# Kernel tuning notes

Measured on AMD Instinct MI355X. Metric: run time of the kernel, lower is better.

The kernel has to match this reference:

```python
import jax, jax.numpy as jnp
import numpy as np

B, L, D, OUT, EXP = 4, 4096, 128, 55, 2
D2 = 2 * D

def _ln(x, g, b):
    m = jnp.mean(x, axis=-1, keepdims=True)
    v = jnp.mean((x - m) ** 2, axis=-1, keepdims=True)
    return (x - m) / jnp.sqrt(v + 1e-5) * g + b

def setup_inputs() -> dict:
    key = jax.random.key(0)
    ks = iter(jax.random.split(key, 32))
    w = lambda shape: jax.random.normal(next(ks), shape, jnp.float32) * 0.02
    inp = {
        'x1': jax.random.normal(next(ks), (B, L, D), jnp.float32),
        'x2': jax.random.normal(next(ks), (B, L, D), jnp.float32),
        'ln1_g': jnp.ones((D,)), 'ln1_b': jnp.zeros((D,)),
        'ln2_g': jnp.ones((D,)), 'ln2_b': jnp.zeros((D,)),
        'Wq': w((D, D)), 'bq': jnp.zeros((D,)),
        'Wv1': w((D, D)), 'bv1': jnp.zeros((D,)),
        'Wk': w((D, D)), 'bk': jnp.zeros((D,)),
        'Wv2': w((D, D)), 'bv2': jnp.zeros((D,)),
        'Wp1': w((D, D)), 'bp1': jnp.zeros((D,)),
        'Wp2': w((D, D)), 'bp2': jnp.zeros((D,)),
        'lnf_g': jnp.ones((D2,)), 'lnf_b': jnp.zeros((D2,)),
        'Wf1': w((D2, EXP * D2)), 'bf1': jnp.zeros((EXP * D2,)),
        'Wf2': w((EXP * D2, D2)), 'bf2': jnp.zeros((D2,)),
        'ln3_g': jnp.ones((D2,)), 'ln3_b': jnp.zeros((D2,)),
        'Wo': w((D2, OUT)), 'bo': jnp.zeros((OUT,)),
    }
    return inp

def reference(x1, x2, ln1_g, ln1_b, ln2_g, ln2_b, Wq, bq, Wv1, bv1, Wk, bk,
              Wv2, bv2, Wp1, bp1, Wp2, bp2, lnf_g, lnf_b, Wf1, bf1, Wf2, bf2,
              ln3_g, ln3_b, Wo, bo):
    res1, res2 = x1, x2
    x1n = _ln(x1, ln1_g, ln1_b)
    x2n = _ln(x2, ln2_g, ln2_b)
    q1 = x1n @ Wq + bq        # [B,L,D]
    v1 = x1n @ Wv1 + bv1
    k2 = x2n @ Wk + bk
    v2 = x2n @ Wv2 + bv2
    # faithful to torch: energy = einsum('bqd,bkd->bqk', keys2, queries1)
    energy = jnp.einsum('bqd,bkd->bqk', k2, q1)
    att = jax.nn.softmax(energy / jnp.sqrt(jnp.float32(D)), axis=-1)  # [B,L,L]
    out1 = jnp.einsum('bal,blv->bav', att, v1) @ Wp1 + bp1
    out2 = jnp.einsum('bal,blv->bav', att, v2) @ Wp2 + bp2
    y1 = out1 + res1
    y2 = out2 + res2
    x = jnp.concatenate([y1, y2], axis=-1)  # [B,L,2D]
    res = x
    h = _ln(x, lnf_g, lnf_b)
    h = jax.nn.gelu(h @ Wf1 + bf1, approximate=False) @ Wf2 + bf2
    x = _ln(h + res, ln3_g, ln3_b)
    return x @ Wo + bo  # [B,L,OUT]
```

## Files before the change

### kernel.cpp

```cpp
#include <hip/hip_runtime.h>
#include <hip/hip_fp16.h>

typedef _Float16 half8 __attribute__((ext_vector_type(8)));
typedef float f32x4 __attribute__((ext_vector_type(4)));
typedef long lng2 __attribute__((ext_vector_type(2)));

#define B_   4
#define L_   4096
#define D_   128
#define M_   (B_*L_)
#define D2_  256
#define H_   512
#define OUT_ 55

__device__ __forceinline__ f32x4 mfma16(half8 a, half8 b, f32x4 c) {
    return __builtin_amdgcn_mfma_f32_16x16x32_f16(a, b, c, 0, 0, 0);
}
__device__ __forceinline__ f32x4 mfma8(long a, long b, f32x4 c) {
    return __builtin_amdgcn_mfma_f32_16x16x32_fp8_fp8(a, b, c, 0, 0, 0);
}
__device__ __forceinline__ int pk4(float a, float b, float c, float d) {
    int t = __builtin_amdgcn_cvt_pk_fp8_f32(a, b, 0, false);
    return __builtin_amdgcn_cvt_pk_fp8_f32(c, d, t, true);
}
__device__ __forceinline__ float fexp2(float x) { return __builtin_amdgcn_exp2f(x); }

#define KSCL (0.08838834764831845f * 1.4426950408889634f)

#define WQ_OFF   0
#define WV1_OFF  16384
#define WK_OFF   32768
#define WV2_OFF  49152
#define WP1_OFF  65536
#define WP2_OFF  81920
#define WF1_OFF  98304
#define WF2_OFF  229376
#define WO_OFF   360448


__global__ void prep_kernel(const float* Wq, const float* Wv1, const float* Wk,
                            const float* Wv2, const float* Wp1, const float* Wp2,
                            const float* Wf1, const float* Wf2, const float* Wo,
                            _Float16* wsw) {
    int id = blockIdx.y;
    int t  = blockIdx.x * 256 + threadIdx.x;
    const float* src = nullptr; int K = 0, N = 0, Npad = 0, off = 0;
    switch (id) {
        case 0: src = Wq;  K = 128; N = 128; Npad = 128; off = WQ_OFF;  break;
        case 1: src = Wv1; K = 128; N = 128; Npad = 128; off = WV1_OFF; break;
        case 2: src = Wk;  K = 128; N = 128; Npad = 128; off = WK_OFF;  break;
        case 3: src = Wv2; K = 128; N = 128; Npad = 128; off = WV2_OFF; break;
        case 4: src = Wp1; K = 128; N = 128; Npad = 128; off = WP1_OFF; break;
        case 5: src = Wp2; K = 128; N = 128; Npad = 128; off = WP2_OFF; break;
        case 6: src = Wf1; K = 256; N = 512; Npad = 512; off = WF1_OFF; break;
        case 7: src = Wf2; K = 512; N = 256; Npad = 256; off = WF2_OFF; break;
        case 8: src = Wo;  K = 256; N = 55;  Npad = 64;  off = WO_OFF;  break;
        default: return;
    }
    int total = K * Npad;
    if (t >= total) return;
    int k = t / Npad, n = t % Npad;
    float v = (n < N) ? src[k * N + n] : 0.f;
    int s = k >> 5, c = n >> 4, ln = n & 15;
    int q, j;
    if (id == 4 || id == 5) { q = (k >> 2) & 3; j = (k & 3) + (((k >> 4) & 1) << 2); }
    else                    { q = (k >> 3) & 3; j = k & 7; }
    int nc = Npad >> 4;
    wsw[off + ((size_t)((s * nc + c) * 64 + q * 16 + ln)) * 8 + j] = (_Float16)v;
}


__global__ __launch_bounds__(256) void ln_kernel(const float* x1, const float* x2,
        const float* g1, const float* b1, const float* g2, const float* b2,
        _Float16* x1n, _Float16* x2n) {
    int wave = threadIdx.x >> 6, lane = threadIdx.x & 63;
    int token = blockIdx.x * 4 + wave;
    const float* x = blockIdx.y ? x2 : x1;
    const float* g = blockIdx.y ? g2 : g1;
    const float* bb = blockIdx.y ? b2 : b1;
    _Float16* o = blockIdx.y ? x2n : x1n;
    const float* xr = x + (size_t)token * D_;
    float a0 = xr[lane], a1 = xr[lane + 64];
    float s = a0 + a1, s2 = a0 * a0 + a1 * a1;
    #pragma unroll
    for (int off = 1; off < 64; off <<= 1) {
        s += __shfl_xor(s, off);
        s2 += __shfl_xor(s2, off);
    }
    float mean = s * (1.f / 128.f);
    float var = s2 * (1.f / 128.f) - mean * mean;
    float inv = rsqrtf(var + 1e-5f);
    int lt = token >> 4, ln_r = token & 15;
    #pragma unroll
    for (int h = 0; h < 2; h++) {
        int col = lane + h * 64;
        float v = (h ? a1 : a0);
        float out = (v - mean) * inv * g[col] + bb[col];
        int ss = col >> 5, q = (col >> 3) & 3, j = col & 7;
        o[((size_t)((lt * 4 + ss) * 64 + q * 16 + ln_r)) * 8 + j] = (_Float16)out;
    }
}

__global__ __launch_bounds__(256) void proj_kernel(const _Float16* x1n, const _Float16* x2n,
        const _Float16* wsw, const float* bq, const float* bv1, const float* bk,
        const float* bv2, _Float16* q1, _Float16* k2, unsigned char* vsw8) {
    int g = blockIdx.y;
    const _Float16* A = (g < 2) ? x1n : x2n;
    const _Float16* Bw = wsw + g * 16384;
    const float* bias = (g == 0) ? bq : (g == 1) ? bv1 : (g == 2) ? bk : bv2;
    int wave = threadIdx.x >> 6, lane = threadIdx.x & 63;
    int quad = lane >> 4, ln = lane & 15;
    int mbase = blockIdx.x * 64 + wave * 16;
    int lt = mbase >> 4;

    half8 a[4];
    #pragma unroll
    for (int s = 0; s < 4; s++)
        a[s] = *(const half8*)(A + ((size_t)((lt * 4 + s) * 64 + lane)) * 8);

    f32x4 acc[8];
    #pragma unroll
    for (int c = 0; c < 8; c++) acc[c] = f32x4{0.f, 0.f, 0.f, 0.f};

    half8 Wc[4], Wn[4];
    #pragma unroll
    for (int s = 0; s < 4; s++)
        Wc[s] = *(const half8*)(Bw + ((size_t)((s * 8 + 0) * 64 + lane)) * 8);
    #pragma unroll
    for (int c = 0; c < 8; c++) {
        int cn = (c < 7) ? c + 1 : 7;
        #pragma unroll
        for (int s = 0; s < 4; s++)
            Wn[s] = *(const half8*)(Bw + ((size_t)((s * 8 + cn) * 64 + lane)) * 8);
        #pragma unroll
        for (int s = 0; s < 4; s++)
            acc[c] = mfma16(a[s], Wc[s], acc[c]);
        #pragma unroll
        for (int s = 0; s < 4; s++) Wc[s] = Wn[s];
    }

    bool isV = (g == 1) || (g == 3);
    if (!isV) {
        float scl = (g == 2) ? KSCL : 1.f;
        _Float16* out = (g == 0) ? q1 : k2;
        #pragma unroll
        for (int c = 0; c < 8; c++) {
            int n = c * 16 + ln;
            float bv = bias[n];
            #pragma unroll
            for (int r = 0; r < 4; r++) {
                int s_o = c >> 1, q_o = ((c & 1) << 1) | (ln >> 3), j = ln & 7;
                out[((size_t)((lt * 4 + s_o) * 64 + q_o * 16 + (quad * 4 + r))) * 8 + j]
                    = (_Float16)((acc[c][r] + bv) * scl);
            }
        }
    } else {
        int cbase = (g == 3) ? 8 : 0;
        int b = mbase >> 12;
        int l0 = (mbase & (L_ - 1)) + quad * 4;
        int sp = l0 >> 6, tt = (l0 >> 4) & 3, q2 = (l0 >> 2) & 3;
        unsigned char* Vb = vsw8 + (size_t)b * (1u << 20);
        #pragma unroll
        for (int c = 0; c < 8; c++) {
            int n = c * 16 + ln;
            float bv = bias[n];
            int pk = pk4(acc[c][0] + bv, acc[c][1] + bv, acc[c][2] + bv, acc[c][3] + bv);
            *(int*)(Vb + (((size_t)(sp * 16 + cbase + c) * 64 + q2 * 16 + ln) * 16 + tt * 4)) = pk;
        }
    }
}

__global__ __launch_bounds__(256) void zero_kernel(float* rowsum) {
    int i = (blockIdx.x * 256 + threadIdx.x) * 4;
    *(f32x4*)(rowsum + i) = f32x4{0.f, 0.f, 0.f, 0.f};
}

__global__ __launch_bounds__(256) void score_kernel(
        const _Float16* __restrict__ q1sw, const _Float16* __restrict__ k2sw,
        unsigned char* __restrict__ pmat8, float* __restrict__ rowsum) {
    int w = threadIdx.x >> 6, lane = threadIdx.x & 63;
    int quad = lane >> 4, ln = lane & 15;
    int b = blockIdx.z;
    int kL0 = blockIdx.y * 128 + (w & 1) * 64;
    int mL0 = blockIdx.x * 128 + (w >> 1) * 64;
    int ltk = ((b << 12) + kL0) >> 4;
    int ltm = ((b << 12) + mL0) >> 4;

    f32x4 acc[4][4];
    #pragma unroll
    for (int i = 0; i < 4; i++)
        #pragma unroll
        for (int j = 0; j < 4; j++) acc[i][j] = f32x4{0.f, 0.f, 0.f, 0.f};

    #pragma unroll
    for (int s = 0; s < 4; s++) {
        half8 a[4], bq[4];
        #pragma unroll
        for (int i = 0; i < 4; i++)
            a[i] = *(const half8*)(q1sw + ((size_t)(((ltk + i) * 4 + s) * 64 + lane)) * 8);
        #pragma unroll
        for (int j = 0; j < 4; j++)
            bq[j] = *(const half8*)(k2sw + ((size_t)(((ltm + j) * 4 + s) * 64 + lane)) * 8);
        #pragma unroll
        for (int i = 0; i < 4; i++)
            #pragma unroll
            for (int j = 0; j < 4; j++)
                acc[i][j] = mfma16(a[i], bq[j], acc[i][j]);
    }

    unsigned char* Pb = pmat8 + (size_t)b * (16u << 20);
    int sp = kL0 >> 6;
    #pragma unroll
    for (int j = 0; j < 4; j++) {
        int4 d;
        float csum = 0.f;
        #pragma unroll
        for (int i = 0; i < 4; i++) {
            float p0 = fexp2(acc[i][j][0]);
            float p1 = fexp2(acc[i][j][1]);
            float p2 = fexp2(acc[i][j][2]);
            float p3 = fexp2(acc[i][j][3]);
            csum += (p0 + p1) + (p2 + p3);
            ((int*)&d)[i] = pk4(p0, p1, p2, p3);
        }
        csum += __shfl_xor(csum, 16);
        csum += __shfl_xor(csum, 32);
        if (lane < 16)
            atomicAdd(&rowsum[(b << 12) + mL0 + j * 16 + ln], csum);
        int lt = (mL0 >> 4) + j;
        *(int4*)(Pb + (((size_t)(lt * 64 + sp)) * 64 + lane) * 16) = d;
    }
}

__global__ __launch_bounds__(256) void pv_kernel(
        const unsigned char* __restrict__ pmat8, const unsigned char* __restrict__ vsw8,
        const float* __restrict__ rowsum,
        _Float16* __restrict__ att1, _Float16* __restrict__ att2) {
    int w = threadIdx.x >> 6, lane = threadIdx.x & 63;
    int quad = lane >> 4, ln = lane & 15;
    int rowG0 = blockIdx.x * 32;
    int b = rowG0 >> 12;
    int lt0 = (rowG0 & (L_ - 1)) >> 4;
    const unsigned char* Pb = pmat8 + (size_t)b * (16u << 20);
    const unsigned char* Vb = vsw8 + (size_t)b * (1u << 20);

    f32x4 acc[4][2];
    #pragma unroll
    for (int i = 0; i < 4; i++)
        #pragma unroll
        for (int c = 0; c < 2; c++) acc[i][c] = f32x4{0.f, 0.f, 0.f, 0.f};

    lng2 Vf[2][4], Pf[2][2];
    #pragma unroll
    for (int p = 0; p < 2; p++) {
        #pragma unroll
        for (int i = 0; i < 4; i++)
            Vf[p][i] = *(const lng2*)(Vb + (((size_t)(p * 16 + w * 4 + i)) * 64 + lane) * 16);
        #pragma unroll
        for (int c = 0; c < 2; c++)
            Pf[p][c] = *(const lng2*)(Pb + (((size_t)((lt0 + c) * 64 + p)) * 64 + lane) * 16);
    }

    #define PVSTEP(buf, sp) do {                                                     \
        int spn = ((sp) + 2 < 64) ? (sp) + 2 : 63;                                   \
        lng2 Vn[4], Pn[2];                                                           \
        _Pragma("unroll")                                                            \
        for (int i = 0; i < 4; i++)                                                  \
            Vn[i] = *(const lng2*)(Vb + (((size_t)(spn * 16 + w * 4 + i)) * 64 + lane) * 16); \
        _Pragma("unroll")                                                            \
        for (int c = 0; c < 2; c++)                                                  \
            Pn[c] = *(const lng2*)(Pb + (((size_t)((lt0 + c) * 64 + spn)) * 64 + lane) * 16); \
        _Pragma("unroll")                                                            \
        for (int i = 0; i < 4; i++)                                                  \
            _Pragma("unroll")                                                        \
            for (int c = 0; c < 2; c++) {                                            \
                acc[i][c] = mfma8(Vf[buf][i].x, Pf[buf][c].x, acc[i][c]);             \
                acc[i][c] = mfma8(Vf[buf][i].y, Pf[buf][c].y, acc[i][c]);             \
            }                                                                        \
        _Pragma("unroll")                                                            \
        for (int i = 0; i < 4; i++) Vf[buf][i] = Vn[i];                              \
        _Pragma("unroll")                                                            \
        for (int c = 0; c < 2; c++) Pf[buf][c] = Pn[c];                              \
    } while (0)

    for (int sp = 0; sp < 64; sp += 2) {
        PVSTEP(0, sp);
        PVSTEP(1, sp + 1);
    }
    #undef PVSTEP

    _Float16* att = (w >= 2) ? att2 : att1;
    #pragma unroll
    for (int c = 0; c < 2; c++) {
        float inv = 1.f / rowsum[rowG0 + c * 16 + ln];
        int lt = (rowG0 >> 4) + c;
        #pragma unroll
        for (int sl = 0; sl < 2; sl++) {
            half8 v;
            #pragma unroll
            for (int r = 0; r < 4; r++) {
                v[r]     = (_Float16)(acc[2 * sl][c][r] * inv);
                v[r + 4] = (_Float16)(acc[2 * sl + 1][c][r] * inv);
            }
            int s = (w & 1) * 2 + sl;
            *(half8*)(att + ((size_t)((lt * 4 + s) * 64 + lane)) * 8) = v;
        }
    }
}

__global__ __launch_bounds__(256) void attn_out_kernel(const _Float16* att1, const _Float16* att2,
        const _Float16* wsw, const float* bp1, const float* bp2,
        const float* x1, const float* x2, const float* lnf_g, const float* lnf_b,
        _Float16* res, _Float16* xn) {
    int wave = threadIdx.x >> 6, lane = threadIdx.x & 63;
    int quad = lane >> 4, ln = lane & 15;
    int mbase = blockIdx.x * 64 + wave * 16;
    int lt = mbase >> 4;
    const _Float16* Wp1 = wsw + WP1_OFF;
    const _Float16* Wp2 = wsw + WP2_OFF;

    half8 a1[4], a2[4];
    #pragma unroll
    for (int s = 0; s < 4; s++) {
        a1[s] = *(const half8*)(att1 + ((size_t)((lt * 4 + s) * 64 + lane)) * 8);
        a2[s] = *(const half8*)(att2 + ((size_t)((lt * 4 + s) * 64 + lane)) * 8);
    }
    f32x4 y1[8], y2[8];
    #pragma unroll
    for (int c = 0; c < 8; c++) { y1[c] = f32x4{0,0,0,0}; y2[c] = f32x4{0,0,0,0}; }

    half8 W1c[4], W2c[4], W1n[4], W2n[4];
    #pragma unroll
    for (int s = 0; s < 4; s++) {
        W1c[s] = *(const half8*)(Wp1 + ((size_t)((s * 8 + 0) * 64 + lane)) * 8);
        W2c[s] = *(const half8*)(Wp2 + ((size_t)((s * 8 + 0) * 64 + lane)) * 8);
    }
    #pragma unroll
    for (int c = 0; c < 8; c++) {
        int cn = (c < 7) ? c + 1 : 7;
        #pragma unroll
        for (int s = 0; s < 4; s++) {
            W1n[s] = *(const half8*)(Wp1 + ((size_t)((s * 8 + cn) * 64 + lane)) * 8);
            W2n[s] = *(const half8*)(Wp2 + ((size_t)((s * 8 + cn) * 64 + lane)) * 8);
        }
        #pragma unroll
        for (int s = 0; s < 4; s++) {
            y1[c] = mfma16(a1[s], W1c[s], y1[c]);
            y2[c] = mfma16(a2[s], W2c[s], y2[c]);
        }
        #pragma unroll
        for (int s = 0; s < 4; s++) { W1c[s] = W1n[s]; W2c[s] = W2n[s]; }
    }

    #pragma unroll
    for (int c = 0; c < 8; c++) {
        int n = c * 16 + ln;
        float b1v = bp1[n], b2v = bp2[n];
        #pragma unroll
        for (int r = 0; r < 4; r++) {
            int m = mbase + quad * 4 + r;
            y1[c][r] += b1v + x1[(size_t)m * D_ + n];
            y2[c][r] += b2v + x2[(size_t)m * D_ + n];
        }
    }
    float sum[4] = {0,0,0,0}, sq[4] = {0,0,0,0};
    #pragma unroll
    for (int c = 0; c < 8; c++)
        #pragma unroll
        for (int r = 0; r < 4; r++) {
            sum[r] += y1[c][r] + y2[c][r];
            sq[r]  += y1[c][r] * y1[c][r] + y2[c][r] * y2[c][r];
        }
    #pragma unroll
    for (int off = 1; off < 16; off <<= 1)
        #pragma unroll
        for (int r = 0; r < 4; r++) { sum[r] += __shfl_xor(sum[r], off); sq[r] += __shfl_xor(sq[r], off); }
    #pragma unroll
    for (int r = 0; r < 4; r++) {
        float mean = sum[r] * (1.f / 256.f);
        float var = sq[r] * (1.f / 256.f) - mean * mean;
        float inv = rsqrtf(var + 1e-5f);
        int m = mbase + quad * 4 + r;
        int lt_m = m >> 4;
        #pragma unroll
        for (int c = 0; c < 8; c++) {
            int n = c * 16 + ln;
            res[(size_t)m * D2_ + n]       = (_Float16)y1[c][r];
            res[(size_t)m * D2_ + 128 + n] = (_Float16)y2[c][r];
            float yn1 = (y1[c][r] - mean) * inv * lnf_g[n] + lnf_b[n];
            float yn2 = (y2[c][r] - mean) * inv * lnf_g[128 + n] + lnf_b[128 + n];
            int s_x = n >> 5, q_x = (n >> 3) & 3, j = n & 7;
            xn[((size_t)((lt_m * 8 + s_x) * 64 + q_x * 16 + (m & 15))) * 8 + j] = (_Float16)yn1;
            int n2 = 128 + n;
            int s_y = n2 >> 5, q_y = (n2 >> 3) & 3, j2 = n2 & 7;
            xn[((size_t)((lt_m * 8 + s_y) * 64 + q_y * 16 + (m & 15))) * 8 + j2] = (_Float16)yn2;
        }
    }
}

__global__ __launch_bounds__(256) void ffn1_kernel(const _Float16* xn, const _Float16* wsw,
        const float* bf1, _Float16* h) {
    int wave = threadIdx.x >> 6, lane = threadIdx.x & 63;
    int quad = lane >> 4, ln = lane & 15;
    int mbase = blockIdx.x * 64 + wave * 16;
    int lt = mbase >> 4;
    int nt = blockIdx.y;
    const _Float16* W = wsw + WF1_OFF;

    half8 a[8];
    #pragma unroll
    for (int s = 0; s < 8; s++)
        a[s] = *(const half8*)(xn + ((size_t)((lt * 8 + s) * 64 + lane)) * 8);

    f32x4 acc[8];
    #pragma unroll
    for (int c = 0; c < 8; c++) acc[c] = f32x4{0,0,0,0};

    half8 Wc[8], Wn[8];
    #pragma unroll
    for (int s = 0; s < 8; s++)
        Wc[s] = *(const half8*)(W + ((size_t)((s * 32 + nt * 8) * 64 + lane)) * 8);
    #pragma unroll
    for (int c = 0; c < 8; c++) {
        int cn = (c < 7) ? c + 1 : 7;
        #pragma unroll
        for (int s = 0; s < 8; s++)
            Wn[s] = *(const half8*)(W + ((size_t)((s * 32 + nt * 8 + cn) * 64 + lane)) * 8);
        #pragma unroll
        for (int s = 0; s < 8; s++)
            acc[c] = mfma16(a[s], Wc[s], acc[c]);
        #pragma unroll
        for (int s = 0; s < 8; s++) Wc[s] = Wn[s];
    }
    #pragma unroll
    for (int c = 0; c < 8; c++) {
        int n = nt * 128 + c * 16 + ln;
        float bv = bf1[n];
        int s_h = n >> 5, q_h = (n >> 3) & 3, j = n & 7;
        #pragma unroll
        for (int r = 0; r < 4; r++) {
            float v = acc[c][r] + bv;
            float u = 0.7978845608f * (v + 0.044715f * v * v * v);
            float e = fexp2(-2.8853900818f * u);
            float ge = v * __builtin_amdgcn_rcpf(1.f + e);
            h[((size_t)((lt * 16 + s_h) * 64 + q_h * 16 + (quad * 4 + r))) * 8 + j] = (_Float16)ge;
        }
    }
}

__global__ __launch_bounds__(256) void ffn2_kernel(const _Float16* h, const _Float16* wsw,
        const float* bf2, const _Float16* res, const float* g3, const float* b3, _Float16* xn2) {
    __shared__ float sst[2][16][2][2];
    int w = threadIdx.x >> 6, lane = threadIdx.x & 63;
    int quad = lane >> 4, ln = lane & 15;
    int rt = w & 1, nh = w >> 1;
    int mb = blockIdx.x * 32 + rt * 16;
    int lt = mb >> 4;
    const _Float16* W = wsw + WF2_OFF;

    f32x4 acc[8];
    #pragma unroll
    for (int c = 0; c < 8; c++) acc[c] = f32x4{0,0,0,0};

    half8 aC, aN;
    half8 Wc[8], Wn[8];
    aC = *(const half8*)(h + ((size_t)((lt * 16 + 0) * 64 + lane)) * 8);
    #pragma unroll
    for (int c = 0; c < 8; c++)
        Wc[c] = *(const half8*)(W + ((size_t)((0 * 16 + nh * 8 + c) * 64 + lane)) * 8);

    #pragma unroll
    for (int s = 0; s < 16; s++) {
        int sn = (s < 15) ? s + 1 : 15;
        aN = *(const half8*)(h + ((size_t)((lt * 16 + sn) * 64 + lane)) * 8);
        #pragma unroll
        for (int c = 0; c < 8; c++)
            Wn[c] = *(const half8*)(W + ((size_t)((sn * 16 + nh * 8 + c) * 64 + lane)) * 8);
        #pragma unroll
        for (int c = 0; c < 8; c++)
            acc[c] = mfma16(aC, Wc[c], acc[c]);
        aC = aN;
        #pragma unroll
        for (int c = 0; c < 8; c++) Wc[c] = Wn[c];
    }

    float y[8][4];
    float psum[4] = {0,0,0,0}, psq[4] = {0,0,0,0};
    #pragma unroll
    for (int c = 0; c < 8; c++) {
        int n = nh * 128 + c * 16 + ln;
        float bv = bf2[n];
        #pragma unroll
        for (int r = 0; r < 4; r++) {
            int m = mb + quad * 4 + r;
            float v = acc[c][r] + bv + (float)res[(size_t)m * D2_ + n];
            y[c][r] = v; psum[r] += v; psq[r] += v * v;
        }
    }
    #pragma unroll
    for (int off = 1; off < 16; off <<= 1)
        #pragma unroll
        for (int r = 0; r < 4; r++) { psum[r] += __shfl_xor(psum[r], off); psq[r] += __shfl_xor(psq[r], off); }
    if (ln == 0)
        #pragma unroll
        for (int r = 0; r < 4; r++) { sst[rt][quad * 4 + r][nh][0] = psum[r]; sst[rt][quad * 4 + r][nh][1] = psq[r]; }
    __syncthreads();
    #pragma unroll
    for (int r = 0; r < 4; r++) {
        float su = sst[rt][quad * 4 + r][0][0] + sst[rt][quad * 4 + r][1][0];
        float sq = sst[rt][quad * 4 + r][0][1] + sst[rt][quad * 4 + r][1][1];
        float mean = su * (1.f / 256.f);
        float var = sq * (1.f / 256.f) - mean * mean;
        float invs = rsqrtf(var + 1e-5f);
        #pragma unroll
        for (int c = 0; c < 8; c++) {
            int n = nh * 128 + c * 16 + ln;
            float yn = (y[c][r] - mean) * invs * g3[n] + b3[n];
            int s_x = n >> 5, q_x = (n >> 3) & 3, j = n & 7;
            xn2[((size_t)((lt * 8 + s_x) * 64 + q_x * 16 + (quad * 4 + r))) * 8 + j] = (_Float16)yn;
        }
    }
}

__global__ __launch_bounds__(256) void out_kernel(const _Float16* xn2, const _Float16* wsw,
        const float* bo, float* out) {
    __shared__ f32x4 pc[2][4][64];
    int w = threadIdx.x >> 6, lane = threadIdx.x & 63;
    int quad = lane >> 4, ln = lane & 15;
    int rt = w & 1, kh = w >> 1;
    int mb = blockIdx.x * 32 + rt * 16;
    int lt = mb >> 4;
    const _Float16* W = wsw + WO_OFF;

    f32x4 acc[4];
    #pragma unroll
    for (int c = 0; c < 4; c++) acc[c] = f32x4{0,0,0,0};
    #pragma unroll
    for (int ss = 0; ss < 4; ss++) {
        int s = kh * 4 + ss;
        half8 a = *(const half8*)(xn2 + ((size_t)((lt * 8 + s) * 64 + lane)) * 8);
        #pragma unroll
        for (int c = 0; c < 4; c++)
            acc[c] = mfma16(a, *(const half8*)(W + ((size_t)((s * 4 + c) * 64 + lane)) * 8), acc[c]);
    }
    if (kh == 1)
        #pragma unroll
        for (int c = 0; c < 4; c++) pc[rt][c][lane] = acc[c];
    __syncthreads();
    if (kh == 0) {
        #pragma unroll
        for (int c = 0; c < 4; c++) {
            f32x4 p = pc[rt][c][lane];
            int n = c * 16 + ln;
            if (n < OUT_) {
                float bv = bo[n];
                #pragma unroll
                for (int r = 0; r < 4; r++)
                    out[(size_t)(mb + quad * 4 + r) * OUT_ + n] = acc[c][r] + p[r] + bv;
            }
        }
    }
}

extern "C" void kernel_launch(void* const* d_in, const int* in_sizes, int n_in,
                              void* d_out, int out_size, void* d_ws, size_t ws_size,
                              hipStream_t stream) {
    const float* x1    = (const float*)d_in[0];
    const float* x2    = (const float*)d_in[1];
    const float* ln1_g = (const float*)d_in[2];
    const float* ln1_b = (const float*)d_in[3];
    const float* ln2_g = (const float*)d_in[4];
    const float* ln2_b = (const float*)d_in[5];
    const float* Wq    = (const float*)d_in[6];
    const float* bq    = (const float*)d_in[7];
    const float* Wv1   = (const float*)d_in[8];
    const float* bv1   = (const float*)d_in[9];
    const float* Wk    = (const float*)d_in[10];
    const float* bk    = (const float*)d_in[11];
    const float* Wv2   = (const float*)d_in[12];
    const float* bv2   = (const float*)d_in[13];
    const float* Wp1   = (const float*)d_in[14];
    const float* bp1   = (const float*)d_in[15];
    const float* Wp2   = (const float*)d_in[16];
    const float* bp2   = (const float*)d_in[17];
    const float* lnf_g = (const float*)d_in[18];
    const float* lnf_b = (const float*)d_in[19];
    const float* Wf1   = (const float*)d_in[20];
    const float* bf1   = (const float*)d_in[21];
    const float* Wf2   = (const float*)d_in[22];
    const float* bf2   = (const float*)d_in[23];
    const float* ln3_g = (const float*)d_in[24];
    const float* ln3_b = (const float*)d_in[25];
    const float* Wo    = (const float*)d_in[26];
    const float* bo    = (const float*)d_in[27];
    float* out = (float*)d_out;

    char* ws = (char*)d_ws;
    const size_t MB = 1 << 20;
    _Float16* q1sw   = (_Float16*)(ws + 0 * MB);
    _Float16* k2sw   = (_Float16*)(ws + 4 * MB);
    unsigned char* vsw8 = (unsigned char*)(ws + 8 * MB);
    _Float16* att1   = (_Float16*)(ws + 12 * MB);
    _Float16* att2   = (_Float16*)(ws + 16 * MB);
    _Float16* x1n    = (_Float16*)(ws + 20 * MB);
    _Float16* x2n    = (_Float16*)(ws + 24 * MB);
    _Float16* wsw    = (_Float16*)(ws + 28 * MB);
    float*    rowsum = (float*)   (ws + 29 * MB);
    _Float16* res    = (_Float16*)(ws + 30 * MB);
    _Float16* xn     = (_Float16*)(ws + 46 * MB);
    _Float16* h      = (_Float16*)(ws + 54 * MB);
    _Float16* xn2    = (_Float16*)(ws + 70 * MB);
    unsigned char* pmat8 = (unsigned char*)(ws + 78 * MB);

    prep_kernel<<<dim3(512, 9), 256, 0, stream>>>(Wq, Wv1, Wk, Wv2, Wp1, Wp2, Wf1, Wf2, Wo, wsw);
    ln_kernel<<<dim3(M_ / 4, 2), 256, 0, stream>>>(x1, x2, ln1_g, ln1_b, ln2_g, ln2_b, x1n, x2n);
    proj_kernel<<<dim3(M_ / 64, 4), 256, 0, stream>>>(x1n, x2n, wsw, bq, bv1, bk, bv2,
                                                      q1sw, k2sw, vsw8);
    zero_kernel<<<dim3(16), 256, 0, stream>>>(rowsum);
    score_kernel<<<dim3(32, 32, 4), 256, 0, stream>>>(q1sw, k2sw, pmat8, rowsum);
    pv_kernel<<<dim3(M_ / 32), 256, 0, stream>>>(pmat8, vsw8, rowsum, att1, att2);
    attn_out_kernel<<<dim3(M_ / 64), 256, 0, stream>>>(att1, att2, wsw, bp1, bp2,
                                                       x1, x2, lnf_g, lnf_b, res, xn);
    ffn1_kernel<<<dim3(M_ / 64, 4), 256, 0, stream>>>(xn, wsw, bf1, h);
    ffn2_kernel<<<dim3(M_ / 32), 256, 0, stream>>>(h, wsw, bf2, res, ln3_g, ln3_b, xn2);
    out_kernel<<<dim3(M_ / 32), 256, 0, stream>>>(xn2, wsw, bo, out);
}
```

Measured before the change: 249.6 us.

## Split PV reduction across wave halves and split attn_out by stream

pv_kernel now launches 512 threads per block. Two groups of four waves each cover half of the key dimension, and the partial accumulators are combined through shared memory before normalization and the store. attn_out_kernel assigns each wave a single stream (att1 or att2) over 16 rows, doubling the grid, and combines the layernorm statistics across waves through shared memory. Both changes aim to raise parallelism and occupancy on the memory-bound stages, at the cost of extra LDS traffic and a block-wide barrier.

```diff
diff --git a/kernel.cpp b/kernel.cpp
--- a/kernel.cpp
+++ b/kernel.cpp
@@ -232,17 +232,21 @@
     }
 }
 
-__global__ __launch_bounds__(256) void pv_kernel(
+__global__ __launch_bounds__(512) void pv_kernel(
         const unsigned char* __restrict__ pmat8, const unsigned char* __restrict__ vsw8,
         const float* __restrict__ rowsum,
         _Float16* __restrict__ att1, _Float16* __restrict__ att2) {
+    __shared__ f32x4 part[4][2][4][64];
     int w = threadIdx.x >> 6, lane = threadIdx.x & 63;
     int quad = lane >> 4, ln = lane & 15;
+    int wc = w & 3, kh = w >> 2;
     int rowG0 = blockIdx.x * 32;
     int b = rowG0 >> 12;
     int lt0 = (rowG0 & (L_ - 1)) >> 4;
     const unsigned char* Pb = pmat8 + (size_t)b * (16u << 20);
     const unsigned char* Vb = vsw8 + (size_t)b * (1u << 20);
+    int c0 = wc * 4;
+    int sp0 = kh * 32;
 
     f32x4 acc[4][2];
     #pragma unroll
@@ -255,18 +259,18 @@
     for (int p = 0; p < 2; p++) {
         #pragma unroll
         for (int i = 0; i < 4; i++)
-            Vf[p][i] = *(const lng2*)(Vb + (((size_t)(p * 16 + w * 4 + i)) * 64 + lane) * 16);
+            Vf[p][i] = *(const lng2*)(Vb + (((size_t)((sp0 + p) * 16 + c0 + i)) * 64 + lane) * 16);
         #pragma unroll
         for (int c = 0; c < 2; c++)
-            Pf[p][c] = *(const lng2*)(Pb + (((size_t)((lt0 + c) * 64 + p)) * 64 + lane) * 16);
-    }
-
-    #define PVSTEP(buf, sp) do {                                                     \
-        int spn = ((sp) + 2 < 64) ? (sp) + 2 : 63;                                   \
+            Pf[p][c] = *(const lng2*)(Pb + (((size_t)((lt0 + c) * 64 + sp0 + p)) * 64 + lane) * 16);
+    }
+
+    #define PVSTEP(buf, ii) do {                                                     \
+        int spn = sp0 + ((((ii) + 2) < 32) ? (ii) + 2 : 31);                         \
         lng2 Vn[4], Pn[2];                                                           \
         _Pragma("unroll")                                                            \
         for (int i = 0; i < 4; i++)                                                  \
-            Vn[i] = *(const lng2*)(Vb + (((size_t)(spn * 16 + w * 4 + i)) * 64 + lane) * 16); \
+            Vn[i] = *(const lng2*)(Vb + (((size_t)(spn * 16 + c0 + i)) * 64 + lane) * 16); \
         _Pragma("unroll")                                                            \
         for (int c = 0; c < 2; c++)                                                  \
             Pn[c] = *(const lng2*)(Pb + (((size_t)((lt0 + c) * 64 + spn)) * 64 + lane) * 16); \
@@ -283,27 +287,43 @@
         for (int c = 0; c < 2; c++) Pf[buf][c] = Pn[c];                              \
     } while (0)
 
-    for (int sp = 0; sp < 64; sp += 2) {
-        PVSTEP(0, sp);
-        PVSTEP(1, sp + 1);
+    for (int ii = 0; ii < 32; ii += 2) {
+        PVSTEP(0, ii);
+        PVSTEP(1, ii + 1);
     }
     #undef PVSTEP
 
-    _Float16* att = (w >= 2) ? att2 : att1;
-    #pragma unroll
-    for (int c = 0; c < 2; c++) {
-        float inv = 1.f / rowsum[rowG0 + c * 16 + ln];
-        int lt = (rowG0 >> 4) + c;
-        #pragma unroll
-        for (int sl = 0; sl < 2; sl++) {
-            half8 v;
+    if (kh == 1) {
+        #pragma unroll
+        for (int i = 0; i < 4; i++)
             #pragma unroll
-            for (int r = 0; r < 4; r++) {
-                v[r]     = (_Float16)(acc[2 * sl][c][r] * inv);
-                v[r + 4] = (_Float16)(acc[2 * sl + 1][c][r] * inv);
+            for (int c = 0; c < 2; c++)
+                part[wc][c][i][lane] = acc[i][c];
+    }
+    __syncthreads();
+    if (kh == 0) {
+        #pragma unroll
+        for (int i = 0; i < 4; i++)
+            #pragma unroll
+            for (int c = 0; c < 2; c++)
+                acc[i][c] += part[wc][c][i][lane];
+
+        _Float16* att = (wc >= 2) ? att2 : att1;
+        #pragma unroll
+        for (int c = 0; c < 2; c++) {
+            float inv = 1.f / rowsum[rowG0 + c * 16 + ln];
+            int lt = (rowG0 >> 4) + c;
+            #pragma unroll
+            for (int sl = 0; sl < 2; sl++) {
+                half8 v;
+                #pragma unroll
+                for (int r = 0; r < 4; r++) {
+                    v[r]     = (_Float16)(acc[2 * sl][c][r] * inv);
+                    v[r + 4] = (_Float16)(acc[2 * sl + 1][c][r] * inv);
+                }
+                int s = (wc & 1) * 2 + sl;
+                *(half8*)(att + ((size_t)((lt * 4 + s) * 64 + lane)) * 8) = v;
             }
-            int s = (w & 1) * 2 + sl;
-            *(half8*)(att + ((size_t)((lt * 4 + s) * 64 + lane)) * 8) = v;
         }
     }
 }
@@ -312,88 +332,82 @@
         const _Float16* wsw, const float* bp1, const float* bp2,
         const float* x1, const float* x2, const float* lnf_g, const float* lnf_b,
         _Float16* res, _Float16* xn) {
-    int wave = threadIdx.x >> 6, lane = threadIdx.x & 63;
+    __shared__ float sst[2][16][2][2];
+    int w = threadIdx.x >> 6, lane = threadIdx.x & 63;
     int quad = lane >> 4, ln = lane & 15;
-    int mbase = blockIdx.x * 64 + wave * 16;
+    int rt = w & 1, st = w >> 1;
+    int mbase = blockIdx.x * 32 + rt * 16;
     int lt = mbase >> 4;
-    const _Float16* Wp1 = wsw + WP1_OFF;
-    const _Float16* Wp2 = wsw + WP2_OFF;
-
-    half8 a1[4], a2[4];
-    #pragma unroll
-    for (int s = 0; s < 4; s++) {
-        a1[s] = *(const half8*)(att1 + ((size_t)((lt * 4 + s) * 64 + lane)) * 8);
-        a2[s] = *(const half8*)(att2 + ((size_t)((lt * 4 + s) * 64 + lane)) * 8);
-    }
-    f32x4 y1[8], y2[8];
-    #pragma unroll
-    for (int c = 0; c < 8; c++) { y1[c] = f32x4{0,0,0,0}; y2[c] = f32x4{0,0,0,0}; }
-
-    half8 W1c[4], W2c[4], W1n[4], W2n[4];
-    #pragma unroll
-    for (int s = 0; s < 4; s++) {
-        W1c[s] = *(const half8*)(Wp1 + ((size_t)((s * 8 + 0) * 64 + lane)) * 8);
-        W2c[s] = *(const half8*)(Wp2 + ((size_t)((s * 8 + 0) * 64 + lane)) * 8);
-    }
+    const _Float16* att = st ? att2 : att1;
+    const _Float16* Wp = wsw + (st ? WP2_OFF : WP1_OFF);
+    const float* bp = st ? bp2 : bp1;
+    const float* xres = st ? x2 : x1;
+
+    half8 a[4];
+    #pragma unroll
+    for (int s = 0; s < 4; s++)
+        a[s] = *(const half8*)(att + ((size_t)((lt * 4 + s) * 64 + lane)) * 8);
+
+    f32x4 y[8];
+    #pragma unroll
+    for (int c = 0; c < 8; c++) y[c] = f32x4{0,0,0,0};
+
+    half8 Wc[4], Wn[4];
+    #pragma unroll
+    for (int s = 0; s < 4; s++)
+        Wc[s] = *(const half8*)(Wp + ((size_t)((s * 8 + 0) * 64 + lane)) * 8);
     #pragma unroll
     for (int c = 0; c < 8; c++) {
         int cn = (c < 7) ? c + 1 : 7;
         #pragma unroll
-        for (int s = 0; s < 4; s++) {
-            W1n[s] = *(const half8*)(Wp1 + ((size_t)((s * 8 + cn) * 64 + lane)) * 8);
-            W2n[s] = *(const half8*)(Wp2 + ((size_t)((s * 8 + cn) * 64 + lane)) * 8);
-        }
-        #pragma unroll
-        for (int s = 0; s < 4; s++) {
-            y1[c] = mfma16(a1[s], W1c[s], y1[c]);
-            y2[c] = mfma16(a2[s], W2c[s], y2[c]);
-        }
-        #pragma unroll
-        for (int s = 0; s < 4; s++) { W1c[s] = W1n[s]; W2c[s] = W2n[s]; }
-    }
-
+        for (int s = 0; s < 4; s++)
+            Wn[s] = *(const half8*)(Wp + ((size_t)((s * 8 + cn) * 64 + lane)) * 8);
+        #pragma unroll
+        for (int s = 0; s < 4; s++)
+            y[c] = mfma16(a[s], Wc[s], y[c]);
+        #pragma unroll
+        for (int s = 0; s < 4; s++) Wc[s] = Wn[s];
+    }
+
+    float psum[4] = {0,0,0,0}, psq[4] = {0,0,0,0};
     #pragma unroll
     for (int c = 0; c < 8; c++) {
         int n = c * 16 + ln;
-        float b1v = bp1[n], b2v = bp2[n];
+        float bv = bp[n];
         #pragma unroll
         for (int r = 0; r < 4; r++) {
             int m = mbase + quad * 4 + r;
-            y1[c][r] += b1v + x1[(size_t)m * D_ + n];
-            y2[c][r] += b2v + x2[(size_t)m * D_ + n];
-        }
-    }
-    float sum[4] = {0,0,0,0}, sq[4] = {0,0,0,0};
-    #pragma unroll
-    for (int c = 0; c < 8; c++)
+            float v = y[c][r] + bv + xres[(size_t)m * D_ + n];
+            y[c][r] = v; psum[r] += v; psq[r] += v * v;
+        }
+    }
+    #pragma unroll
+    for (int off = 1; off < 16; off <<= 1)
+        #pragma unroll
+        for (int r = 0; r < 4; r++) { psum[r] += __shfl_xor(psum[r], off); psq[r] += __shfl_xor(psq[r], off); }
+    if (ln == 0)
         #pragma unroll
         for (int r = 0; r < 4; r++) {
-            sum[r] += y1[c][r] + y2[c][r];
-            sq[r]  += y1[c][r] * y1[c][r] + y2[c][r] * y2[c][r];
-        }
-    #pragma unroll
-    for (int off = 1; off < 16; off <<= 1)
-        #pragma unroll
-        for (int r = 0; r < 4; r++) { sum[r] += __shfl_xor(sum[r], off); sq[r] += __shfl_xor(sq[r], off); }
+            sst[rt][quad * 4 + r][st][0] = psum[r];
+            sst[rt][quad * 4 + r][st][1] = psq[r];
+        }
+    __syncthreads();
     #pragma unroll
     for (int r = 0; r < 4; r++) {
-        float mean = sum[r] * (1.f / 256.f);
-        float var = sq[r] * (1.f / 256.f) - mean * mean;
+        float su = sst[rt][quad * 4 + r][0][0] + sst[rt][quad * 4 + r][1][0];
+        float sq = sst[rt][quad * 4 + r][0][1] + sst[rt][quad * 4 + r][1][1];
+        float mean = su * (1.f / 256.f);
+        float var = sq * (1.f / 256.f) - mean * mean;
         float inv = rsqrtf(var + 1e-5f);
         int m = mbase + quad * 4 + r;
         int lt_m = m >> 4;
         #pragma unroll
         for (int c = 0; c < 8; c++) {
-            int n = c * 16 + ln;
-            res[(size_t)m * D2_ + n]       = (_Float16)y1[c][r];
-            res[(size_t)m * D2_ + 128 + n] = (_Float16)y2[c][r];
-            float yn1 = (y1[c][r] - mean) * inv * lnf_g[n] + lnf_b[n];
-            float yn2 = (y2[c][r] - mean) * inv * lnf_g[128 + n] + lnf_b[128 + n];
-            int s_x = n >> 5, q_x = (n >> 3) & 3, j = n & 7;
-            xn[((size_t)((lt_m * 8 + s_x) * 64 + q_x * 16 + (m & 15))) * 8 + j] = (_Float16)yn1;
-            int n2 = 128 + n;
-            int s_y = n2 >> 5, q_y = (n2 >> 3) & 3, j2 = n2 & 7;
-            xn[((size_t)((lt_m * 8 + s_y) * 64 + q_y * 16 + (m & 15))) * 8 + j2] = (_Float16)yn2;
+            int colg = st * 128 + c * 16 + ln;
+            res[(size_t)m * D2_ + colg] = (_Float16)y[c][r];
+            float yn = (y[c][r] - mean) * inv * lnf_g[colg] + lnf_b[colg];
+            int s_x = colg >> 5, q_x = (colg >> 3) & 3, j = colg & 7;
+            xn[((size_t)((lt_m * 8 + s_x) * 64 + q_x * 16 + (m & 15))) * 8 + j] = (_Float16)yn;
         }
     }
 }
@@ -618,8 +632,8 @@
                                                       q1sw, k2sw, vsw8);
     zero_kernel<<<dim3(16), 256, 0, stream>>>(rowsum);
     score_kernel<<<dim3(32, 32, 4), 256, 0, stream>>>(q1sw, k2sw, pmat8, rowsum);
-    pv_kernel<<<dim3(M_ / 32), 256, 0, stream>>>(pmat8, vsw8, rowsum, att1, att2);
-    attn_out_kernel<<<dim3(M_ / 64), 256, 0, stream>>>(att1, att2, wsw, bp1, bp2,
+    pv_kernel<<<dim3(M_ / 32), 512, 0, stream>>>(pmat8, vsw8, rowsum, att1, att2);
+    attn_out_kernel<<<dim3(M_ / 32), 256, 0, stream>>>(att1, att2, wsw, bp1, bp2,
                                                        x1, x2, lnf_g, lnf_b, res, xn);
     ffn1_kernel<<<dim3(M_ / 64, 4), 256, 0, stream>>>(xn, wsw, bf1, h);
     ffn2_kernel<<<dim3(M_ / 32), 256, 0, stream>>>(h, wsw, bf2, res, ln3_g, ln3_b, xn2);
```

After: 240.8 us. 1.04x faster.
